# Kernel optimization log

Hardware: AMD Instinct MI355X
Metric: run time of the kernel (lower is better)

## Reference

```python
import jax, jax.numpy as jnp
import numpy as np

H = 16   # num_heads
A = 64   # attn_size
D = 1024 # dims
NEG = -1000000000.0


def setup_inputs() -> dict:
    key = jax.random.key(0)
    k1, k2, k3, k4 = jax.random.split(key, 4)
    B, S = 2, 2048
    qs = jax.random.normal(k1, (B, S, D), dtype=jnp.float32)
    mask = jax.random.randint(k2, (B, S), 0, 2, dtype=jnp.int32)
    Wqkv = jax.random.normal(k3, (D, 3 * H * A), dtype=jnp.float32) * (1.0 / np.sqrt(D))
    Wout = jax.random.normal(k4, (H * A, D), dtype=jnp.float32) * (1.0 / np.sqrt(H * A))
    bout = jnp.zeros((D,), dtype=jnp.float32)
    return {"qs": qs, "mask": mask, "Wqkv": Wqkv, "Wout": Wout, "bout": bout}


def reference(qs, mask, Wqkv, Wout, bout):
    B, S, _ = qs.shape
    qkv = qs @ Wqkv                              # [B,S,3*H*A]
    qkv = qkv.reshape(B, S, 3 * H, A)            # split axis=2 in thirds (TF layout)
    q = jnp.transpose(qkv[:, :, 0:H, :], (0, 2, 1, 3))        # [B,H,S,A]
    k = jnp.transpose(qkv[:, :, H:2 * H, :], (0, 2, 1, 3))    # [B,H,S,A]
    v = jnp.transpose(qkv[:, :, 2 * H:3 * H, :], (0, 2, 1, 3))# [B,H,S,A]
    scores = jnp.einsum('bhqa,bhka->bhqk', q, k) / jnp.sqrt(jnp.float32(A))
    m = mask[:, None, None, :]                   # [B,1,1,S] broadcast over heads, queries
    scores = jnp.where(m == 0, NEG, scores)
    probs = jax.nn.softmax(scores, axis=-1)      # dropout_prob=0 / inference -> identity
    ctx = jnp.einsum('bhqk,bhka->bhqa', probs, v)  # [B,H,S,A]
    ctx = jnp.transpose(ctx, (0, 2, 1, 3)).reshape(B, S, H * A)
    return ctx @ Wout + bout
```

## Files before the change

kernel.cpp:

```cpp
#include <hip/hip_runtime.h>
#include <stdint.h>


typedef unsigned short u16;
typedef u16   u16x4  __attribute__((ext_vector_type(4)));
typedef u16   u16x8  __attribute__((ext_vector_type(8)));
typedef __bf16 bf16x8 __attribute__((ext_vector_type(8)));
typedef float f32x4  __attribute__((ext_vector_type(4)));

#define DEV __device__ __forceinline__

DEV u16 f2bf(float f) {
    uint32_t u = __builtin_bit_cast(uint32_t, f);
    u += 0x7fffu + ((u >> 16) & 1u);
    return (u16)(u >> 16);
}

DEV void async16(const void* g, void* l) {
    __builtin_amdgcn_global_load_lds(
        reinterpret_cast<const uint32_t __attribute__((address_space(1)))*>(
            reinterpret_cast<uintptr_t>(g)),
        reinterpret_cast<uint32_t __attribute__((address_space(3)))*>(
            reinterpret_cast<uintptr_t>(l)),
        16, 0, 0);
}

DEV f32x4 mfma16(bf16x8 a, bf16x8 b, f32x4 c) {
    return __builtin_amdgcn_mfma_f32_16x16x32_bf16(a, b, c, 0, 0, 0);
}


__global__ void k_conv(const float* __restrict__ src, u16* __restrict__ dst) {
    int i = (blockIdx.x * 256 + threadIdx.x) * 4;
    float4 v = *reinterpret_cast<const float4*>(src + i);
    u16x4 o = { f2bf(v.x), f2bf(v.y), f2bf(v.z), f2bf(v.w) };
    *reinterpret_cast<u16x4*>(dst + i) = o;
}

__global__ void k_tconv(const float* __restrict__ src, u16* __restrict__ dst, int R, int C) {
    __shared__ float t[32][33];
    int c0 = blockIdx.x * 32, r0 = blockIdx.y * 32;
    int tx = threadIdx.x, ty = threadIdx.y;
#pragma unroll
    for (int i = 0; i < 4; ++i)
        t[ty + 8 * i][tx] = src[(size_t)(r0 + ty + 8 * i) * C + c0 + tx];
    __syncthreads();
#pragma unroll
    for (int i = 0; i < 4; ++i)
        dst[(size_t)(c0 + ty + 8 * i) * R + r0 + tx] = f2bf(t[tx][ty + 8 * i]);
}

__global__ void k_mask(const int* __restrict__ m, float* __restrict__ b) {
    int i = blockIdx.x * 256 + threadIdx.x;
    b[i] = m[i] ? 0.0f : -1.0e9f;
}


template <bool OUT_BF16, bool HAS_BIAS>
__global__ __launch_bounds__(256, 2) void k_gemm(
    const u16* __restrict__ A, const u16* __restrict__ Bt,
    void* __restrict__ Cv, const float* __restrict__ bias,
    int M, int N, int K)
{
    __shared__ __attribute__((aligned(16))) u16 As[2][128 * 32];
    __shared__ __attribute__((aligned(16))) u16 Bs[2][128 * 32];

    const int tid = threadIdx.x, wave = tid >> 6, lane = tid & 63;
    const int lh = lane & 15, lg = lane >> 4;
    const int nbn = N >> 7;

    const int nwg = gridDim.x;
    const int q8 = nwg >> 3, r8 = nwg & 7;
    const int xcd = blockIdx.x & 7, li = blockIdx.x >> 3;
    const int wg = (xcd < r8 ? xcd * (q8 + 1) : r8 * (q8 + 1) + (xcd - r8) * q8) + li;

    const int m0 = (wg / nbn) * 128, n0 = (wg % nbn) * 128;
    const int wm = wave >> 1, wn = wave & 1;
    const int nk = K >> 5;

    auto stage = [&](int buf, int kt) {
#pragma unroll
        for (int i = 0; i < 2; ++i) {
            int c = (wave * 2 + i) * 64 + lane;
            int row = c >> 2, cc = c & 3;
            int sc = cc ^ (row & 3);
            async16(A  + (size_t)(m0 + row) * K + kt * 32 + sc * 8, &As[buf][(wave * 2 + i) * 512]);
            async16(Bt + (size_t)(n0 + row) * K + kt * 32 + sc * 8, &Bs[buf][(wave * 2 + i) * 512]);
        }
    };

    f32x4 acc[4][4] = {};
    stage(0, 0);
    for (int kt = 0; kt < nk; ++kt) {
        __syncthreads();
        if (kt + 1 < nk) stage((kt + 1) & 1, kt + 1);
        const int buf = kt & 1;
        bf16x8 af[4], bf_[4];
#pragma unroll
        for (int mt = 0; mt < 4; ++mt) {
            int row = wm * 64 + mt * 16 + lh;
            int off = row * 64 + ((lg * 16) ^ ((row & 3) << 4));
            af[mt] = __builtin_bit_cast(bf16x8,
                     *reinterpret_cast<const u16x8*>((const char*)&As[buf][0] + off));
        }
#pragma unroll
        for (int nt = 0; nt < 4; ++nt) {
            int row = wn * 64 + nt * 16 + lh;
            int off = row * 64 + ((lg * 16) ^ ((row & 3) << 4));
            bf_[nt] = __builtin_bit_cast(bf16x8,
                      *reinterpret_cast<const u16x8*>((const char*)&Bs[buf][0] + off));
        }
        __builtin_amdgcn_s_setprio(1);
#pragma unroll
        for (int mt = 0; mt < 4; ++mt)
#pragma unroll
            for (int nt = 0; nt < 4; ++nt)
                acc[mt][nt] = mfma16(af[mt], bf_[nt], acc[mt][nt]);
        __builtin_amdgcn_s_setprio(0);
        __syncthreads();
    }

#pragma unroll
    for (int mt = 0; mt < 4; ++mt)
#pragma unroll
        for (int nt = 0; nt < 4; ++nt) {
            int col = n0 + wn * 64 + nt * 16 + lh;
#pragma unroll
            for (int r = 0; r < 4; ++r) {
                int row = m0 + wm * 64 + mt * 16 + 4 * lg + r;
                float v = acc[mt][nt][r];
                if (HAS_BIAS) v += bias[col];
                if (OUT_BF16) ((u16*)Cv)[(size_t)row * N + col] = f2bf(v);
                else          ((float*)Cv)[(size_t)row * N + col] = v;
            }
        }
}


__global__ __launch_bounds__(512, 4) void k_attn(
    const u16* __restrict__ qkv, const float* __restrict__ biasg, u16* __restrict__ ctx)
{
    __shared__ __attribute__((aligned(16))) u16 Ks[2][64 * 64];
    __shared__ __attribute__((aligned(16))) u16 Vt[2][64 * 72];
    __shared__ __attribute__((aligned(16))) u16 Ps[8 * 16 * 72];

    const int tid = threadIdx.x, wave = tid >> 6, lane = tid & 63;
    const int lh = lane & 15, lg = lane >> 4;

    const int wg = (blockIdx.x & 7) * 64 + (blockIdx.x >> 3);
    const int qt = wg & 15, bh = wg >> 4;
    const int b = bh >> 4, h = bh & 15;

    const u16* qbase = qkv + ((size_t)b * 2048 * 48 + h) * 64;
    const u16* kbase = qkv + ((size_t)b * 2048 * 48 + 16 + h) * 64;
    const u16* vbase = qkv + ((size_t)b * 2048 * 48 + 32 + h) * 64;
    const float* brow = biasg + b * 2048;

    const int srow = wave * 8 + (lane >> 3);
    const int scc  = lane & 7;
    const int ksrc = scc ^ (srow & 7);
    const int vswz = srow ^ (scc << 3);

    bf16x8 qf[2];
    {
        int row = qt * 128 + wave * 16 + lh;
        qf[0] = __builtin_bit_cast(bf16x8,
            *reinterpret_cast<const u16x8*>(qbase + (size_t)row * 3072 + lg * 8));
        qf[1] = __builtin_bit_cast(bf16x8,
            *reinterpret_cast<const u16x8*>(qbase + (size_t)row * 3072 + 32 + lg * 8));
    }

    f32x4 oa[4] = {};
    float lst[4] = {0.0f, 0.0f, 0.0f, 0.0f};

    u16* Pw = &Ps[wave * 16 * 72];

    {
        async16(kbase + (size_t)srow * 3072 + ksrc * 8, &Ks[0][wave * 512]);
        u16x8 v = *reinterpret_cast<const u16x8*>(vbase + (size_t)srow * 3072 + scc * 8);
#pragma unroll
        for (int j = 0; j < 8; ++j) Vt[0][(scc * 8 + j) * 72 + vswz] = v[j];
    }

    for (int kt = 0; kt < 32; ++kt) {
        __syncthreads();
        const int buf = kt & 1;
        if (kt + 1 < 32) {
            async16(kbase + (size_t)((kt + 1) * 64 + srow) * 3072 + ksrc * 8, &Ks[buf ^ 1][wave * 512]);
            u16x8 v = *reinterpret_cast<const u16x8*>(
                vbase + (size_t)((kt + 1) * 64 + srow) * 3072 + scc * 8);
#pragma unroll
            for (int j = 0; j < 8; ++j) Vt[buf ^ 1][(scc * 8 + j) * 72 + vswz] = v[j];
        }

        float biasv[4];
#pragma unroll
        for (int nt = 0; nt < 4; ++nt) biasv[nt] = brow[kt * 64 + nt * 16 + lh];

        f32x4 sa[4] = {};
        __builtin_amdgcn_s_setprio(1);
#pragma unroll
        for (int ks = 0; ks < 2; ++ks) {
            bf16x8 kb[4];
#pragma unroll
            for (int nt = 0; nt < 4; ++nt) {
                int row = nt * 16 + lh;
                int off = row * 64 + (((ks * 4 + lg) ^ (row & 7)) << 3);
                kb[nt] = __builtin_bit_cast(bf16x8,
                         *reinterpret_cast<const u16x8*>(&Ks[buf][off]));
            }
#pragma unroll
            for (int nt = 0; nt < 4; ++nt)
                sa[nt] = mfma16(qf[ks], kb[nt], sa[nt]);
        }
        __builtin_amdgcn_s_setprio(0);

#pragma unroll
        for (int nt = 0; nt < 4; ++nt)
#pragma unroll
            for (int r = 0; r < 4; ++r) {
                float e = __expf(sa[nt][r] * 0.125f + biasv[nt]);
                lst[r] += e;
                Pw[(4 * lg + r) * 72 + nt * 16 + lh] = f2bf(e);
            }

        __builtin_amdgcn_s_setprio(1);
#pragma unroll
        for (int ks = 0; ks < 2; ++ks) {
            bf16x8 pa = __builtin_bit_cast(bf16x8,
                        *reinterpret_cast<const u16x8*>(Pw + lh * 72 + ks * 32 + lg * 8));
            bf16x8 vb[4];
#pragma unroll
            for (int nt = 0; nt < 4; ++nt) {
                int col = nt * 16 + lh;
                int g = (col >> 3) & 7;
                int off = col * 72 + (((ks * 4 + lg) ^ g) << 3);
                vb[nt] = __builtin_bit_cast(bf16x8,
                         *reinterpret_cast<const u16x8*>(&Vt[buf][off]));
            }
#pragma unroll
            for (int nt = 0; nt < 4; ++nt)
                oa[nt] = mfma16(pa, vb[nt], oa[nt]);
        }
        __builtin_amdgcn_s_setprio(0);
    }

#pragma unroll
    for (int r = 0; r < 4; ++r) {
        float s = lst[r];
#pragma unroll
        for (int o = 1; o < 16; o <<= 1) s += __shfl_xor(s, o);
        lst[r] = 1.0f / s;
    }

#pragma unroll
    for (int nt = 0; nt < 4; ++nt)
#pragma unroll
        for (int r = 0; r < 4; ++r) {
            int row = qt * 128 + wave * 16 + 4 * lg + r;
            ctx[(size_t)(b * 2048 + row) * 1024 + h * 64 + nt * 16 + lh] = f2bf(oa[nt][r] * lst[r]);
        }
}


extern "C" void kernel_launch(void* const* d_in, const int* in_sizes, int n_in,
                              void* d_out, int out_size, void* d_ws, size_t ws_size,
                              hipStream_t stream)
{
    const float* qs   = (const float*)d_in[0];
    const int*   mask = (const int*)d_in[1];
    const float* Wqkv = (const float*)d_in[2];
    const float* Wout = (const float*)d_in[3];
    const float* bout = (const float*)d_in[4];
    float* out = (float*)d_out;

    char* ws = (char*)d_ws;
    u16*   qs_bf = (u16*)(ws);
    u16*   WqkvT = (u16*)(ws + 8388608);
    u16*   WoutT = (u16*)(ws + 14680064);
    u16*   qkvb  = (u16*)(ws + 16777216);
    u16*   ctxb  = (u16*)(ws + 41943040);
    float* biasb = (float*)(ws + 50331648);

    k_conv<<<4096, 256, 0, stream>>>(qs, qs_bf);
    k_tconv<<<dim3(96, 32), dim3(32, 8), 0, stream>>>(Wqkv, WqkvT, 1024, 3072);
    k_tconv<<<dim3(32, 32), dim3(32, 8), 0, stream>>>(Wout, WoutT, 1024, 1024);
    k_mask<<<16, 256, 0, stream>>>(mask, biasb);

    k_gemm<true, false><<<768, 256, 0, stream>>>(qs_bf, WqkvT, qkvb, nullptr, 4096, 3072, 1024);
    k_attn<<<512, 512, 0, stream>>>(qkvb, biasb, ctxb);
    k_gemm<false, true><<<256, 256, 0, stream>>>(ctxb, WoutT, out, bout, 4096, 1024, 1024);
}
```

Baseline: 202.4 us.

## Merge prep kernels, widen GEMM to 8 waves, and use exp2 softmax

Fuses the qs conversion and mask-bias kernels into one launch, and both weight transposes into another, cutting launch count. The GEMM moves to 512-thread blocks with 8 waves, each computing smaller 32-wide output tiles, and the output GEMM uses 64-row tiles for more blocks. Attention softmax switches to exp2 with the scale and log2e folded into one FMA, with the mask bias prescaled to match. Smaller per-wave tiles raise occupancy but lower MFMA-to-LDS-load reuse.

```diff
diff --git a/kernel.cpp b/kernel.cpp
--- a/kernel.cpp
+++ b/kernel.cpp
@@ -3,6 +3,7 @@
 
 
 typedef unsigned short u16;
+typedef uint32_t u32;
 typedef u16   u16x4  __attribute__((ext_vector_type(4)));
 typedef u16   u16x8  __attribute__((ext_vector_type(8)));
 typedef __bf16 bf16x8 __attribute__((ext_vector_type(8)));
@@ -11,7 +12,7 @@
 #define DEV __device__ __forceinline__
 
 DEV u16 f2bf(float f) {
-    uint32_t u = __builtin_bit_cast(uint32_t, f);
+    u32 u = __builtin_bit_cast(u32, f);
     u += 0x7fffu + ((u >> 16) & 1u);
     return (u16)(u >> 16);
 }
@@ -30,17 +31,29 @@
 }
 
 
-__global__ void k_conv(const float* __restrict__ src, u16* __restrict__ dst) {
-    int i = (blockIdx.x * 256 + threadIdx.x) * 4;
-    float4 v = *reinterpret_cast<const float4*>(src + i);
-    u16x4 o = { f2bf(v.x), f2bf(v.y), f2bf(v.z), f2bf(v.w) };
-    *reinterpret_cast<u16x4*>(dst + i) = o;
-}
-
-__global__ void k_tconv(const float* __restrict__ src, u16* __restrict__ dst, int R, int C) {
+__global__ void k_prep(const float* __restrict__ qs, u16* __restrict__ qs_bf,
+                       const int* __restrict__ m, float* __restrict__ bias) {
+    int bid = blockIdx.x;
+    if (bid < 4096) {
+        int i = (bid * 256 + threadIdx.x) * 4;
+        float4 v = *reinterpret_cast<const float4*>(qs + i);
+        u16x4 o = { f2bf(v.x), f2bf(v.y), f2bf(v.z), f2bf(v.w) };
+        *reinterpret_cast<u16x4*>(qs_bf + i) = o;
+    } else {
+        int i = (bid - 4096) * 256 + threadIdx.x;
+        bias[i] = m[i] ? 0.0f : -1.442695e9f;
+    }
+}
+
+__global__ void k_tconv(const float* __restrict__ Wqkv, u16* __restrict__ WqkvT,
+                        const float* __restrict__ Wout, u16* __restrict__ WoutT) {
     __shared__ float t[32][33];
-    int c0 = blockIdx.x * 32, r0 = blockIdx.y * 32;
-    int tx = threadIdx.x, ty = threadIdx.y;
+    int bid = blockIdx.x;
+    const float* src; u16* dst; int R, C, bx, by;
+    if (bid < 3072) { src = Wqkv; dst = WqkvT; R = 1024; C = 3072; bx = bid % 96; by = bid / 96; }
+    else { bid -= 3072; src = Wout; dst = WoutT; R = 1024; C = 1024; bx = bid % 32; by = bid / 32; }
+    int c0 = bx * 32, r0 = by * 32;
+    int tx = threadIdx.x & 31, ty = threadIdx.x >> 5;
 #pragma unroll
     for (int i = 0; i < 4; ++i)
         t[ty + 8 * i][tx] = src[(size_t)(r0 + ty + 8 * i) * C + c0 + tx];
@@ -50,19 +63,15 @@
         dst[(size_t)(c0 + ty + 8 * i) * R + r0 + tx] = f2bf(t[tx][ty + 8 * i]);
 }
 
-__global__ void k_mask(const int* __restrict__ m, float* __restrict__ b) {
-    int i = blockIdx.x * 256 + threadIdx.x;
-    b[i] = m[i] ? 0.0f : -1.0e9f;
-}
-
-
-template <bool OUT_BF16, bool HAS_BIAS>
-__global__ __launch_bounds__(256, 2) void k_gemm(
+
+template <int BM, bool OUT_BF16, bool HAS_BIAS>
+__global__ __launch_bounds__(512, 4) void k_gemm(
     const u16* __restrict__ A, const u16* __restrict__ Bt,
     void* __restrict__ Cv, const float* __restrict__ bias,
     int M, int N, int K)
 {
-    __shared__ __attribute__((aligned(16))) u16 As[2][128 * 32];
+    constexpr int MT = BM / 32;
+    __shared__ __attribute__((aligned(16))) u16 As[2][BM * 32];
     __shared__ __attribute__((aligned(16))) u16 Bs[2][128 * 32];
 
     const int tid = threadIdx.x, wave = tid >> 6, lane = tid & 63;
@@ -74,60 +83,58 @@
     const int xcd = blockIdx.x & 7, li = blockIdx.x >> 3;
     const int wg = (xcd < r8 ? xcd * (q8 + 1) : r8 * (q8 + 1) + (xcd - r8) * q8) + li;
 
-    const int m0 = (wg / nbn) * 128, n0 = (wg % nbn) * 128;
-    const int wm = wave >> 1, wn = wave & 1;
+    const int m0 = (wg / nbn) * BM, n0 = (wg % nbn) * 128;
+    const int wm = wave >> 2, wn = wave & 3;
     const int nk = K >> 5;
 
+    const int srow = tid >> 2, scc = tid & 3;
+    const int ssc = scc ^ (srow & 3);
+
     auto stage = [&](int buf, int kt) {
-#pragma unroll
-        for (int i = 0; i < 2; ++i) {
-            int c = (wave * 2 + i) * 64 + lane;
-            int row = c >> 2, cc = c & 3;
-            int sc = cc ^ (row & 3);
-            async16(A  + (size_t)(m0 + row) * K + kt * 32 + sc * 8, &As[buf][(wave * 2 + i) * 512]);
-            async16(Bt + (size_t)(n0 + row) * K + kt * 32 + sc * 8, &Bs[buf][(wave * 2 + i) * 512]);
-        }
+        if (tid < BM * 4)
+            async16(A + (size_t)(m0 + srow) * K + kt * 32 + ssc * 8, &As[buf][tid * 8]);
+        async16(Bt + (size_t)(n0 + srow) * K + kt * 32 + ssc * 8, &Bs[buf][tid * 8]);
     };
 
-    f32x4 acc[4][4] = {};
+    f32x4 acc[MT][2] = {};
     stage(0, 0);
     for (int kt = 0; kt < nk; ++kt) {
         __syncthreads();
         if (kt + 1 < nk) stage((kt + 1) & 1, kt + 1);
         const int buf = kt & 1;
-        bf16x8 af[4], bf_[4];
-#pragma unroll
-        for (int mt = 0; mt < 4; ++mt) {
-            int row = wm * 64 + mt * 16 + lh;
-            int off = row * 64 + ((lg * 16) ^ ((row & 3) << 4));
+        bf16x8 af[MT], bf_[2];
+#pragma unroll
+        for (int mt = 0; mt < MT; ++mt) {
+            int row = wm * (BM / 2) + mt * 16 + lh;
+            int off = row * 32 + ((lg ^ (row & 3)) * 8);
             af[mt] = __builtin_bit_cast(bf16x8,
-                     *reinterpret_cast<const u16x8*>((const char*)&As[buf][0] + off));
-        }
-#pragma unroll
-        for (int nt = 0; nt < 4; ++nt) {
-            int row = wn * 64 + nt * 16 + lh;
-            int off = row * 64 + ((lg * 16) ^ ((row & 3) << 4));
+                     *reinterpret_cast<const u16x8*>(&As[buf][off]));
+        }
+#pragma unroll
+        for (int nt = 0; nt < 2; ++nt) {
+            int row = wn * 32 + nt * 16 + lh;
+            int off = row * 32 + ((lg ^ (row & 3)) * 8);
             bf_[nt] = __builtin_bit_cast(bf16x8,
-                      *reinterpret_cast<const u16x8*>((const char*)&Bs[buf][0] + off));
+                      *reinterpret_cast<const u16x8*>(&Bs[buf][off]));
         }
         __builtin_amdgcn_s_setprio(1);
 #pragma unroll
-        for (int mt = 0; mt < 4; ++mt)
-#pragma unroll
-            for (int nt = 0; nt < 4; ++nt)
+        for (int mt = 0; mt < MT; ++mt)
+#pragma unroll
+            for (int nt = 0; nt < 2; ++nt)
                 acc[mt][nt] = mfma16(af[mt], bf_[nt], acc[mt][nt]);
         __builtin_amdgcn_s_setprio(0);
         __syncthreads();
     }
 
 #pragma unroll
-    for (int mt = 0; mt < 4; ++mt)
-#pragma unroll
-        for (int nt = 0; nt < 4; ++nt) {
-            int col = n0 + wn * 64 + nt * 16 + lh;
+    for (int mt = 0; mt < MT; ++mt)
+#pragma unroll
+        for (int nt = 0; nt < 2; ++nt) {
+            int col = n0 + wn * 32 + nt * 16 + lh;
 #pragma unroll
             for (int r = 0; r < 4; ++r) {
-                int row = m0 + wm * 64 + mt * 16 + 4 * lg + r;
+                int row = m0 + wm * (BM / 2) + mt * 16 + 4 * lg + r;
                 float v = acc[mt][nt][r];
                 if (HAS_BIAS) v += bias[col];
                 if (OUT_BF16) ((u16*)Cv)[(size_t)row * N + col] = f2bf(v);
@@ -215,11 +222,12 @@
         }
         __builtin_amdgcn_s_setprio(0);
 
+        const float SC = 0.1803368801111244f;
 #pragma unroll
         for (int nt = 0; nt < 4; ++nt)
 #pragma unroll
             for (int r = 0; r < 4; ++r) {
-                float e = __expf(sa[nt][r] * 0.125f + biasv[nt]);
+                float e = __builtin_exp2f(fmaf(sa[nt][r], SC, biasv[nt]));
                 lst[r] += e;
                 Pw[(4 * lg + r) * 72 + nt * 16 + lh] = f2bf(e);
             }
@@ -282,12 +290,10 @@
     u16*   ctxb  = (u16*)(ws + 41943040);
     float* biasb = (float*)(ws + 50331648);
 
-    k_conv<<<4096, 256, 0, stream>>>(qs, qs_bf);
-    k_tconv<<<dim3(96, 32), dim3(32, 8), 0, stream>>>(Wqkv, WqkvT, 1024, 3072);
-    k_tconv<<<dim3(32, 32), dim3(32, 8), 0, stream>>>(Wout, WoutT, 1024, 1024);
-    k_mask<<<16, 256, 0, stream>>>(mask, biasb);
-
-    k_gemm<true, false><<<768, 256, 0, stream>>>(qs_bf, WqkvT, qkvb, nullptr, 4096, 3072, 1024);
+    k_prep<<<4112, 256, 0, stream>>>(qs, qs_bf, mask, biasb);
+    k_tconv<<<4096, 256, 0, stream>>>(Wqkv, WqkvT, Wout, WoutT);
+
+    k_gemm<128, true, false><<<768, 512, 0, stream>>>(qs_bf, WqkvT, qkvb, nullptr, 4096, 3072, 1024);
     k_attn<<<512, 512, 0, stream>>>(qkvb, biasb, ctxb);
-    k_gemm<false, true><<<256, 256, 0, stream>>>(ctxb, WoutT, out, bout, 4096, 1024, 1024);
-}
+    k_gemm<64, false, true><<<512, 512, 0, stream>>>(ctxb, WoutT, out, bout, 4096, 1024, 1024);
+}
```

Result: no change. 206.1 us (+1.8%).
